# Performance work log

Measured on AMD Instinct MI355X. Metric: run time of the kernel, lower is better.

The kernel has to match this reference:

```python
import jax, jax.numpy as jnp
import numpy as np

N, E, B = 50000, 640000, 4
H, L = 128, 4
NODE_IN, EDGE_IN, COND_IN, NODE_OUT = 12, 4, 10, 3


def _mlp(x, w1, b1, w2, b2):
    # Linear -> ReLU -> Linear
    return jnp.maximum(x @ w1 + b1, 0.0) @ w2 + b2


def setup_inputs() -> dict:
    key = jax.random.key(0)
    keys = iter(jax.random.split(key, 64))

    def p(*shape):
        fan_in = shape[-2] if len(shape) >= 2 else shape[-1]
        return (jax.random.normal(next(keys), shape, jnp.float32) / np.sqrt(fan_in)).astype(jnp.float32)

    inp = {
        "x": jax.random.normal(next(keys), (N, NODE_IN), jnp.float32),
        "edge_index": jax.random.randint(next(keys), (2, E), 0, N),
        "edge_attr": jax.random.normal(next(keys), (E, EDGE_IN), jnp.float32),
        "conditions": jax.random.normal(next(keys), (B, COND_IN), jnp.float32),
        "batch": jnp.sort(jax.random.randint(next(keys), (N,), 0, B)),
        # encoders
        "enc_node_w1": p(NODE_IN, H), "enc_node_b1": jnp.zeros((H,), jnp.float32),
        "enc_node_w2": p(H, H), "enc_node_b2": jnp.zeros((H,), jnp.float32),
        "enc_edge_w1": p(EDGE_IN, H), "enc_edge_b1": jnp.zeros((H,), jnp.float32),
        "enc_edge_w2": p(H, H), "enc_edge_b2": jnp.zeros((H,), jnp.float32),
        "enc_cond_w1": p(COND_IN, H), "enc_cond_b1": jnp.zeros((H,), jnp.float32),
        "enc_cond_w2": p(H, H), "enc_cond_b2": jnp.zeros((H,), jnp.float32),
        # shared MultiheadAttention: with a single key, softmax weight == 1 per head,
        # so output = out_proj(v_proj(kv)); q/k projections cancel exactly (and have
        # identically zero gradient), so only v/out projections are materialized.
        "attn_wv": p(H, H), "attn_bv": jnp.zeros((H,), jnp.float32),
        "attn_wo": p(H, H), "attn_bo": jnp.zeros((H,), jnp.float32),
        # processor layers (stacked over L)
        "pe_w1": p(L, 4 * H, H), "pe_b1": jnp.zeros((L, H), jnp.float32),
        "pe_w2": p(L, H, H), "pe_b2": jnp.zeros((L, H), jnp.float32),
        "pn_w1": p(L, 3 * H, H), "pn_b1": jnp.zeros((L, H), jnp.float32),
        "pn_w2": p(L, H, H), "pn_b2": jnp.zeros((L, H), jnp.float32),
        # decoder
        "dec_w1": p(H, H), "dec_b1": jnp.zeros((H,), jnp.float32),
        "dec_w2": p(H, NODE_OUT), "dec_b2": jnp.zeros((NODE_OUT,), jnp.float32),
    }
    return inp


def reference(x, edge_index, edge_attr, conditions, batch,
              enc_node_w1, enc_node_b1, enc_node_w2, enc_node_b2,
              enc_edge_w1, enc_edge_b1, enc_edge_w2, enc_edge_b2,
              enc_cond_w1, enc_cond_b1, enc_cond_w2, enc_cond_b2,
              attn_wv, attn_bv, attn_wo, attn_bo,
              pe_w1, pe_b1, pe_w2, pe_b2,
              pn_w1, pn_b1, pn_w2, pn_b2,
              dec_w1, dec_b1, dec_w2, dec_b2):
    n = x.shape[0]
    h = _mlp(x, enc_node_w1, enc_node_b1, enc_node_w2, enc_node_b2)           # [N,H]
    e = _mlp(edge_attr, enc_edge_w1, enc_edge_b1, enc_edge_w2, enc_edge_b2)   # [E,H]
    u = _mlp(conditions, enc_cond_w1, enc_cond_b1, enc_cond_w2, enc_cond_b2)  # [B,H]

    row, col = edge_index[0], edge_index[1]
    u_nodes = u[batch]                                                        # [N,H]
    # single-key cross-attention -> softmax over 1 key == 1 -> out_proj(v_proj(u))
    x_cond = (u_nodes @ attn_wv + attn_bv) @ attn_wo + attn_bo               # [N,H], same every layer
    u_edges = u_nodes[row]                                                    # u[batch[row]]

    for l in range(pe_w1.shape[0]):
        # edge update: cat([src, dest, edge_attr, u[batch_e]]) -> MLP
        e = _mlp(jnp.concatenate([h[row], h[col], e, u_edges], axis=1),
                 pe_w1[l], pe_b1[l], pe_w2[l], pe_b2[l])
        # scatter-add aggregation (index_add on row)
        agg = jax.ops.segment_sum(e, row, num_segments=n)                     # [N,H]
        # node update with residual
        h = h + _mlp(jnp.concatenate([h, agg, x_cond], axis=1),
                     pn_w1[l], pn_b1[l], pn_w2[l], pn_b2[l])

    return _mlp(h, dec_w1, dec_b1, dec_w2, dec_b2)                            # [N,node_out]
```

## Files before the change

### kernel.cpp

```cpp
#include <hip/hip_runtime.h>
#include <cstddef>

#define NN 50000
#define NNP 50048
#define NE 640000
#define NB 4
#define H  128
#define NL 4
#define TE 64

typedef unsigned int u32;
typedef unsigned short u16;
typedef __attribute__((ext_vector_type(8))) short bf16x8;
typedef __attribute__((ext_vector_type(4))) float f32x4;

__device__ __forceinline__ float bf2f(u16 s) {
    union { u32 u; float f; } v; v.u = ((u32)s) << 16; return v.f;
}
__device__ __forceinline__ u16 f2bf(float f) {
    union { float f; u32 u; } v; v.f = f;
    u32 u = v.u;
    u += 0x7FFF + ((u >> 16) & 1);
    return (u16)(u >> 16);
}
__device__ __forceinline__ void unpack8(uint4 raw, float* d) {
    d[0] = bf2f(raw.x & 0xFFFF); d[1] = bf2f(raw.x >> 16);
    d[2] = bf2f(raw.y & 0xFFFF); d[3] = bf2f(raw.y >> 16);
    d[4] = bf2f(raw.z & 0xFFFF); d[5] = bf2f(raw.z >> 16);
    d[6] = bf2f(raw.w & 0xFFFF); d[7] = bf2f(raw.w >> 16);
}
__device__ __forceinline__ uint4 pack8(const float* s) {
    uint4 pk;
    pk.x = (u32)f2bf(s[0]) | ((u32)f2bf(s[1]) << 16);
    pk.y = (u32)f2bf(s[2]) | ((u32)f2bf(s[3]) << 16);
    pk.z = (u32)f2bf(s[4]) | ((u32)f2bf(s[5]) << 16);
    pk.w = (u32)f2bf(s[6]) | ((u32)f2bf(s[7]) << 16);
    return pk;
}
__device__ __forceinline__ bf16x8 ld_f32_bf8(const float* __restrict__ p) {
    const float4 a = *(const float4*)p;
    const float4 b = *(const float4*)(p + 4);
    bf16x8 r;
    r[0] = (short)f2bf(a.x); r[1] = (short)f2bf(a.y);
    r[2] = (short)f2bf(a.z); r[3] = (short)f2bf(a.w);
    r[4] = (short)f2bf(b.x); r[5] = (short)f2bf(b.y);
    r[6] = (short)f2bf(b.z); r[7] = (short)f2bf(b.w);
    return r;
}

__global__ __launch_bounds__(256) void k_zero(float* __restrict__ p, int n4) {
    const int i = blockIdx.x * 256 + threadIdx.x;
    if (i < n4) ((float4*)p)[i] = make_float4(0.f, 0.f, 0.f, 0.f);
}

__global__ __launch_bounds__(256) void k_hist(const int* __restrict__ rowi,
                                              u32* __restrict__ cnt) {
    const int i = blockIdx.x * 256 + threadIdx.x;
    if (i < NE) atomicAdd(&cnt[rowi[i]], 1u);
}

__global__ __launch_bounds__(1024) void k_scan(u32* __restrict__ cnt) {
    __shared__ u32 part[1024];
    const int t = threadIdx.x;
    const int CHUNK = (NN + 1023) / 1024;
    const int lo = t * CHUNK;
    const int hi = (lo + CHUNK < NN) ? lo + CHUNK : NN;
    u32 s = 0;
    for (int i = lo; i < hi; ++i) s += cnt[i];
    part[t] = s;
    __syncthreads();
    for (int ofs = 1; ofs < 1024; ofs <<= 1) {
        const u32 v = (t >= ofs) ? part[t - ofs] : 0u;
        __syncthreads();
        part[t] += v;
        __syncthreads();
    }
    u32 run = (t == 0) ? 0u : part[t - 1];
    for (int i = lo; i < hi; ++i) { const u32 c = cnt[i]; cnt[i] = run; run += c; }
}

__global__ __launch_bounds__(256) void k_scatter(const int* __restrict__ rowi,
                                                 const int* __restrict__ coli,
                                                 u32* __restrict__ off,
                                                 int* __restrict__ permS,
                                                 int* __restrict__ rowS,
                                                 int* __restrict__ colS) {
    const int i = blockIdx.x * 256 + threadIdx.x;
    if (i < NE) {
        const int r = rowi[i];
        const u32 p = atomicAdd(&off[r], 1u);
        permS[p] = i; rowS[p] = r; colS[p] = coli[i];
    }
}

__global__ __launch_bounds__(256) void k_prep(
    const float* __restrict__ pe_w1, const float* __restrict__ pe_w2,
    const float* __restrict__ pn_w1, const float* __restrict__ pn_w2,
    const float* __restrict__ ew2,   const float* __restrict__ nw2,
    const float* __restrict__ dw1,
    u16* __restrict__ W1t, u16* __restrict__ W2t,
    u16* __restrict__ WaT, u16* __restrict__ WbT,
    u16* __restrict__ Wn1aT, u16* __restrict__ Wn1bT, u16* __restrict__ Wn2T,
    u16* __restrict__ W2et, u16* __restrict__ W2nt, u16* __restrict__ W1dt) {
    const int li = blockIdx.x;
    const float* src; u16* dst;
    switch (blockIdx.y) {
        case 0: src = pe_w1 + ((size_t)li * 512 + 256) * H; dst = W1t  + (size_t)li * H * H; break;
        case 1: src = pe_w2 + (size_t)li * H * H;           dst = W2t  + (size_t)li * H * H; break;
        case 2: src = pe_w1 + (size_t)li * 512 * H;         dst = WaT  + (size_t)li * H * H; break;
        case 3: src = pe_w1 + ((size_t)li * 512 + 128) * H; dst = WbT  + (size_t)li * H * H; break;
        case 4: src = pn_w1 + (size_t)li * 384 * H;         dst = Wn1aT + (size_t)li * H * H; break;
        case 5: src = pn_w1 + ((size_t)li * 384 + 128) * H; dst = Wn1bT + (size_t)li * H * H; break;
        case 6: src = pn_w2 + (size_t)li * H * H;           dst = Wn2T + (size_t)li * H * H; break;
        default:
            if (li == 0)      { src = ew2; dst = W2et; }
            else if (li == 1) { src = nw2; dst = W2nt; }
            else if (li == 2) { src = dw1; dst = W1dt; }
            else return;
            break;
    }
    for (int idx = threadIdx.x; idx < H * H; idx += 256) {
        const int n = idx >> 7, k = idx & 127;
        dst[idx] = f2bf(src[(size_t)k * H + n]);
    }
}

__global__ __launch_bounds__(128) void k_small(
    const float* __restrict__ cond,
    const float* __restrict__ ecw1, const float* __restrict__ ecb1,
    const float* __restrict__ ecw2, const float* __restrict__ ecb2,
    const float* __restrict__ wv, const float* __restrict__ bv,
    const float* __restrict__ wo, const float* __restrict__ bo,
    const float* __restrict__ pe_w1, const float* __restrict__ pe_b1,
    const float* __restrict__ pn_w1, const float* __restrict__ pn_b1,
    float* __restrict__ cbat, float* __restrict__ nbat) {
    __shared__ float tmp[NB][H];
    __shared__ float uL[NB][H];
    __shared__ float xcL[NB][H];
    const int t = threadIdx.x;
    for (int b = 0; b < NB; ++b) {
        float a = ecb1[t];
        for (int k = 0; k < 10; ++k) a = fmaf(cond[b * 10 + k], ecw1[k * H + t], a);
        tmp[b][t] = fmaxf(a, 0.f);
    }
    __syncthreads();
    for (int b = 0; b < NB; ++b) {
        float a = ecb2[t];
        for (int k = 0; k < H; ++k) a = fmaf(tmp[b][k], ecw2[k * H + t], a);
        uL[b][t] = a;
    }
    __syncthreads();
    for (int b = 0; b < NB; ++b) {
        float a = bv[t];
        for (int k = 0; k < H; ++k) a = fmaf(uL[b][k], wv[k * H + t], a);
        tmp[b][t] = a;
    }
    __syncthreads();
    for (int b = 0; b < NB; ++b) {
        float a = bo[t];
        for (int k = 0; k < H; ++k) a = fmaf(tmp[b][k], wo[k * H + t], a);
        xcL[b][t] = a;
    }
    __syncthreads();
    for (int l = 0; l < NL; ++l) {
        const float* w1u = pe_w1 + ((size_t)l * 512 + 384) * H;
        for (int b = 0; b < NB; ++b) {
            float a = pe_b1[l * H + t];
            for (int k = 0; k < H; ++k) a = fmaf(uL[b][k], w1u[k * H + t], a);
            cbat[(l * NB + b) * H + t] = a;
        }
        const float* w1x = pn_w1 + ((size_t)l * 384 + 256) * H;
        for (int b = 0; b < NB; ++b) {
            float a = pn_b1[l * H + t];
            for (int k = 0; k < H; ++k) a = fmaf(xcL[b][k], w1x[k * H + t], a);
            nbat[(l * NB + b) * H + t] = a;
        }
    }
}

__global__ __launch_bounds__(256) void k_enc_e_mfma(
    const float* __restrict__ ea,
    const int* __restrict__ permS,
    const float* __restrict__ w1, const float* __restrict__ b1,
    const u16* __restrict__ W2et, const float* __restrict__ b2,
    u16* __restrict__ e) {
    __shared__ float SI[TE][H + 4];
    const int t = threadIdx.x;
    const long long e0 = (long long)blockIdx.x * TE;
    const int w = t >> 6, l = t & 63;
    const int m16 = l & 15, g = l >> 4;
    const int row = w * 16 + m16;

    const int src = permS[e0 + row];
    const float4 av = *(const float4*)&ea[(size_t)src * 4];

    bf16x8 afrag[4];
#pragma unroll
    for (int ks = 0; ks < 4; ++ks) {
        const int c0 = ks * 32 + g * 8;
        float hv[8];
        {
            const float4 ba = *(const float4*)&b1[c0];
            const float4 bb = *(const float4*)&b1[c0 + 4];
            hv[0] = ba.x; hv[1] = ba.y; hv[2] = ba.z; hv[3] = ba.w;
            hv[4] = bb.x; hv[5] = bb.y; hv[6] = bb.z; hv[7] = bb.w;
        }
#pragma unroll
        for (int k = 0; k < 4; ++k) {
            const float s = (k == 0) ? av.x : (k == 1) ? av.y : (k == 2) ? av.z : av.w;
            const float4 wa = *(const float4*)&w1[k * H + c0];
            const float4 wb = *(const float4*)&w1[k * H + c0 + 4];
            hv[0] = fmaf(s, wa.x, hv[0]); hv[1] = fmaf(s, wa.y, hv[1]);
            hv[2] = fmaf(s, wa.z, hv[2]); hv[3] = fmaf(s, wa.w, hv[3]);
            hv[4] = fmaf(s, wb.x, hv[4]); hv[5] = fmaf(s, wb.y, hv[5]);
            hv[6] = fmaf(s, wb.z, hv[6]); hv[7] = fmaf(s, wb.w, hv[7]);
        }
#pragma unroll
        for (int j = 0; j < 8; ++j) afrag[ks][j] = (short)f2bf(fmaxf(hv[j], 0.f));
    }

    f32x4 acc[8];
#pragma unroll
    for (int nt = 0; nt < 8; ++nt) {
        const float bb = b2[nt * 16 + m16];
        acc[nt][0] = bb; acc[nt][1] = bb; acc[nt][2] = bb; acc[nt][3] = bb;
    }
#pragma unroll
    for (int ks = 0; ks < 4; ++ks) {
#pragma unroll
        for (int nt = 0; nt < 8; ++nt) {
            const bf16x8 bfr =
                *(const bf16x8*)&W2et[(size_t)(nt * 16 + m16) * H + ks * 32 + g * 8];
            acc[nt] = __builtin_amdgcn_mfma_f32_16x16x32_bf16(afrag[ks], bfr, acc[nt], 0, 0, 0);
        }
    }

#pragma unroll
    for (int nt = 0; nt < 8; ++nt)
#pragma unroll
        for (int j = 0; j < 4; ++j)
            SI[w * 16 + g * 4 + j][nt * 16 + m16] = acc[nt][j];
    __syncthreads();
    for (int u = t; u < TE * 16; u += 256) {
        const int j = u >> 4, c8 = (u & 15) * 8;
        *(uint4*)&e[(size_t)(e0 + j) * H + c8] = pack8(&SI[j][c8]);
    }
}

__global__ __launch_bounds__(256) void k_enc_n_mfma(
    const float* __restrict__ x,
    const float* __restrict__ w1, const float* __restrict__ b1,
    const u16* __restrict__ W2nt, const float* __restrict__ b2,
    float* __restrict__ h) {
    __shared__ float SI[TE][H + 4];
    const int t = threadIdx.x;
    const long long n0 = (long long)blockIdx.x * TE;
    const int w = t >> 6, l = t & 63;
    const int m16 = l & 15, g = l >> 4;
    const int row = w * 16 + m16;
    const long long nr = (n0 + row < NN) ? (n0 + row) : (NN - 1);

    float av[12];
    {
        const float4 a0 = *(const float4*)&x[nr * 12];
        const float4 a1 = *(const float4*)&x[nr * 12 + 4];
        const float4 a2 = *(const float4*)&x[nr * 12 + 8];
        av[0] = a0.x; av[1] = a0.y; av[2] = a0.z; av[3] = a0.w;
        av[4] = a1.x; av[5] = a1.y; av[6] = a1.z; av[7] = a1.w;
        av[8] = a2.x; av[9] = a2.y; av[10] = a2.z; av[11] = a2.w;
    }

    bf16x8 afrag[4];
#pragma unroll
    for (int ks = 0; ks < 4; ++ks) {
        const int c0 = ks * 32 + g * 8;
        float hv[8];
        {
            const float4 ba = *(const float4*)&b1[c0];
            const float4 bb = *(const float4*)&b1[c0 + 4];
            hv[0] = ba.x; hv[1] = ba.y; hv[2] = ba.z; hv[3] = ba.w;
            hv[4] = bb.x; hv[5] = bb.y; hv[6] = bb.z; hv[7] = bb.w;
        }
#pragma unroll
        for (int k = 0; k < 12; ++k) {
            const float s = av[k];
            const float4 wa = *(const float4*)&w1[k * H + c0];
            const float4 wb = *(const float4*)&w1[k * H + c0 + 4];
            hv[0] = fmaf(s, wa.x, hv[0]); hv[1] = fmaf(s, wa.y, hv[1]);
            hv[2] = fmaf(s, wa.z, hv[2]); hv[3] = fmaf(s, wa.w, hv[3]);
            hv[4] = fmaf(s, wb.x, hv[4]); hv[5] = fmaf(s, wb.y, hv[5]);
            hv[6] = fmaf(s, wb.z, hv[6]); hv[7] = fmaf(s, wb.w, hv[7]);
        }
#pragma unroll
        for (int j = 0; j < 8; ++j) afrag[ks][j] = (short)f2bf(fmaxf(hv[j], 0.f));
    }

    f32x4 acc[8];
#pragma unroll
    for (int nt = 0; nt < 8; ++nt) {
        const float bb = b2[nt * 16 + m16];
        acc[nt][0] = bb; acc[nt][1] = bb; acc[nt][2] = bb; acc[nt][3] = bb;
    }
#pragma unroll
    for (int ks = 0; ks < 4; ++ks) {
#pragma unroll
        for (int nt = 0; nt < 8; ++nt) {
            const bf16x8 bfr =
                *(const bf16x8*)&W2nt[(size_t)(nt * 16 + m16) * H + ks * 32 + g * 8];
            acc[nt] = __builtin_amdgcn_mfma_f32_16x16x32_bf16(afrag[ks], bfr, acc[nt], 0, 0, 0);
        }
    }

#pragma unroll
    for (int nt = 0; nt < 8; ++nt)
#pragma unroll
        for (int j = 0; j < 4; ++j)
            SI[w * 16 + g * 4 + j][nt * 16 + m16] = acc[nt][j];
    __syncthreads();
    for (int u = t; u < TE * H / 4; u += 256) {
        const int j = u >> 5, c4 = (u & 31) * 4;
        *(float4*)&h[(size_t)(n0 + j) * H + c4] = *(const float4*)&SI[j][c4];
    }
}

__global__ __launch_bounds__(256) void k_gemm_dual_mfma(
    const float* __restrict__ h,
    const u16* __restrict__ WaT, const u16* __restrict__ WbT,
    u16* __restrict__ Ca, u16* __restrict__ Cb) {
    __shared__ u16 SI[TE][H + 8];
    const int t = threadIdx.x;
    const long long n0 = (long long)blockIdx.x * TE;
    const int w = t >> 6, l = t & 63;
    const int m16 = l & 15, g = l >> 4;
    const int row = w * 16 + m16;

    bf16x8 afrag[4];
    {
        const float* hp = h + (size_t)(n0 + row) * H + g * 8;
#pragma unroll
        for (int ks = 0; ks < 4; ++ks) afrag[ks] = ld_f32_bf8(hp + ks * 32);
    }

    f32x4 accA[8], accB[8];
#pragma unroll
    for (int nt = 0; nt < 8; ++nt) {
        accA[nt][0] = 0.f; accA[nt][1] = 0.f; accA[nt][2] = 0.f; accA[nt][3] = 0.f;
        accB[nt][0] = 0.f; accB[nt][1] = 0.f; accB[nt][2] = 0.f; accB[nt][3] = 0.f;
    }
#pragma unroll
    for (int ks = 0; ks < 4; ++ks) {
#pragma unroll
        for (int nt = 0; nt < 8; ++nt) {
            const size_t off = (size_t)(nt * 16 + m16) * H + ks * 32 + g * 8;
            const bf16x8 ba = *(const bf16x8*)&WaT[off];
            const bf16x8 bb = *(const bf16x8*)&WbT[off];
            accA[nt] = __builtin_amdgcn_mfma_f32_16x16x32_bf16(afrag[ks], ba, accA[nt], 0, 0, 0);
            accB[nt] = __builtin_amdgcn_mfma_f32_16x16x32_bf16(afrag[ks], bb, accB[nt], 0, 0, 0);
        }
    }

#pragma unroll
    for (int s = 0; s < 2; ++s) {
        __syncthreads();
#pragma unroll
        for (int nt = 0; nt < 8; ++nt)
#pragma unroll
            for (int j = 0; j < 4; ++j)
                SI[w * 16 + g * 4 + j][nt * 16 + m16] =
                    f2bf(s ? accB[nt][j] : accA[nt][j]);
        __syncthreads();
        u16* C = s ? Cb : Ca;
        for (int u = t; u < TE * 16; u += 256) {
            const int j = u >> 4, c8 = (u & 15) * 8;
            *(uint4*)&C[(size_t)(n0 + j) * H + c8] = *(const uint4*)&SI[j][c8];
        }
    }
}

template <bool WRITE_E>
__global__ __launch_bounds__(256) void k_edge_mfma(
    const u16* __restrict__ hA, const u16* __restrict__ hB,
    const float* __restrict__ cbatl,
    const u16* __restrict__ W1t, const u16* __restrict__ W2t,
    const float* __restrict__ b2,
    const int* __restrict__ rowS, const int* __restrict__ colS,
    const int* __restrict__ batch,
    u16* __restrict__ e, float* __restrict__ agg) {
    __shared__ u16 SI[TE][H + 8];
    __shared__ int rL[TE], cL[TE], bL[TE];
    const int t = threadIdx.x;
    const long long e0 = (long long)blockIdx.x * TE;
    const int w = t >> 6, l = t & 63;
    const int m16 = l & 15, g = l >> 4;

    bf16x8 afrag[4];
    {
        const u16* ep = e + (size_t)(e0 + w * 16 + m16) * H + g * 8;
#pragma unroll
        for (int ks = 0; ks < 4; ++ks) afrag[ks] = *(const bf16x8*)(ep + ks * 32);
    }

    if (t < TE) {
        const int r = rowS[e0 + t];
        rL[t] = r; cL[t] = colS[e0 + t]; bL[t] = batch[r];
    }
    __syncthreads();

    for (int u = t; u < TE * 16; u += 256) {
        const int j = u >> 4, c8 = (u & 15) * 8;
        float va[8], vb[8], sm[8];
        unpack8(*(const uint4*)&hA[(size_t)rL[j] * H + c8], va);
        unpack8(*(const uint4*)&hB[(size_t)cL[j] * H + c8], vb);
        const float* cb = &cbatl[bL[j] * H + c8];
#pragma unroll
        for (int q = 0; q < 8; ++q) sm[q] = va[q] + vb[q] + cb[q];
        *(uint4*)&SI[j][c8] = pack8(sm);
    }
    __syncthreads();

    f32x4 acc[8];
#pragma unroll
    for (int nt = 0; nt < 8; ++nt) {
#pragma unroll
        for (int j = 0; j < 4; ++j)
            acc[nt][j] = bf2f(SI[w * 16 + g * 4 + j][nt * 16 + m16]);
#pragma unroll
        for (int ks = 0; ks < 4; ++ks) {
            const bf16x8 bfr =
                *(const bf16x8*)&W1t[(size_t)(nt * 16 + m16) * H + ks * 32 + g * 8];
            acc[nt] = __builtin_amdgcn_mfma_f32_16x16x32_bf16(afrag[ks], bfr, acc[nt], 0, 0, 0);
        }
    }
    __syncthreads();

#pragma unroll
    for (int nt = 0; nt < 8; ++nt)
#pragma unroll
        for (int j = 0; j < 4; ++j)
            SI[w * 16 + g * 4 + j][nt * 16 + m16] = f2bf(fmaxf(acc[nt][j], 0.f));
    __syncthreads();

    f32x4 acc2[8];
#pragma unroll
    for (int nt = 0; nt < 8; ++nt) {
        const float bb = b2[nt * 16 + m16];
        acc2[nt][0] = bb; acc2[nt][1] = bb; acc2[nt][2] = bb; acc2[nt][3] = bb;
    }
#pragma unroll
    for (int ks = 0; ks < 4; ++ks) {
        const bf16x8 a2 = *(const bf16x8*)&SI[w * 16 + m16][ks * 32 + g * 8];
#pragma unroll
        for (int nt = 0; nt < 8; ++nt) {
            const bf16x8 bfr =
                *(const bf16x8*)&W2t[(size_t)(nt * 16 + m16) * H + ks * 32 + g * 8];
            acc2[nt] = __builtin_amdgcn_mfma_f32_16x16x32_bf16(a2, bfr, acc2[nt], 0, 0, 0);
        }
    }

    if (WRITE_E) {
        __syncthreads();
#pragma unroll
        for (int nt = 0; nt < 8; ++nt)
#pragma unroll
            for (int j = 0; j < 4; ++j)
                SI[w * 16 + g * 4 + j][nt * 16 + m16] = f2bf(acc2[nt][j]);
        __syncthreads();
        for (int u = t; u < TE * 16; u += 256) {
            const int j = u >> 4, c8 = (u & 15) * 8;
            *(uint4*)&e[(size_t)(e0 + j) * H + c8] = *(const uint4*)&SI[j][c8];
        }
    }

    {
        const int base = w * 16 + g * 4;
        const int r0 = rL[base], r1 = rL[base + 1], r2 = rL[base + 2], r3 = rL[base + 3];
#pragma unroll
        for (int nt = 0; nt < 8; ++nt) {
            const int c = nt * 16 + m16;
            float s = acc2[nt][0];
            int prev = r0;
            if (r1 == prev) s += acc2[nt][1];
            else { atomicAdd(&agg[(size_t)prev * H + c], s); s = acc2[nt][1]; prev = r1; }
            if (r2 == prev) s += acc2[nt][2];
            else { atomicAdd(&agg[(size_t)prev * H + c], s); s = acc2[nt][2]; prev = r2; }
            if (r3 == prev) s += acc2[nt][3];
            else { atomicAdd(&agg[(size_t)prev * H + c], s); s = acc2[nt][3]; prev = r3; }
            atomicAdd(&agg[(size_t)prev * H + c], s);
        }
    }
}

__global__ __launch_bounds__(256) void k_node_mfma(
    const u16* __restrict__ Wn1aT, const u16* __restrict__ Wn1bT,
    const u16* __restrict__ Wn2T, const float* __restrict__ bn2,
    const float* __restrict__ nbatl, const int* __restrict__ batch,
    const float* __restrict__ agg, float* __restrict__ h) {
    __shared__ float SI[TE][H + 4];
    __shared__ float NBl[NB][H];
    __shared__ int bL[TE];
    const int t = threadIdx.x;
    const long long n0 = (long long)blockIdx.x * TE;
    if (t < TE) {
        const long long n = n0 + t;
        bL[t] = batch[n < NN ? n : (NN - 1)];
    }
    for (int i = t; i < NB * H; i += 256) ((float*)NBl)[i] = nbatl[i];

    const int w = t >> 6, l = t & 63;
    const int m16 = l & 15, g = l >> 4;
    const int row = w * 16 + m16;

    bf16x8 afrag[4];
    {
        const float* hp = h + (size_t)(n0 + row) * H + g * 8;
#pragma unroll
        for (int ks = 0; ks < 4; ++ks) afrag[ks] = ld_f32_bf8(hp + ks * 32);
    }
    __syncthreads();

    f32x4 acc[8];
#pragma unroll
    for (int nt = 0; nt < 8; ++nt)
#pragma unroll
        for (int j = 0; j < 4; ++j)
            acc[nt][j] = NBl[bL[w * 16 + g * 4 + j]][nt * 16 + m16];

#pragma unroll
    for (int ks = 0; ks < 4; ++ks)
#pragma unroll
        for (int nt = 0; nt < 8; ++nt) {
            const bf16x8 bfr =
                *(const bf16x8*)&Wn1aT[(size_t)(nt * 16 + m16) * H + ks * 32 + g * 8];
            acc[nt] = __builtin_amdgcn_mfma_f32_16x16x32_bf16(afrag[ks], bfr, acc[nt], 0, 0, 0);
        }

    {
        const float* ap = agg + (size_t)(n0 + row) * H + g * 8;
#pragma unroll
        for (int ks = 0; ks < 4; ++ks) afrag[ks] = ld_f32_bf8(ap + ks * 32);
    }
#pragma unroll
    for (int ks = 0; ks < 4; ++ks)
#pragma unroll
        for (int nt = 0; nt < 8; ++nt) {
            const bf16x8 bfr =
                *(const bf16x8*)&Wn1bT[(size_t)(nt * 16 + m16) * H + ks * 32 + g * 8];
            acc[nt] = __builtin_amdgcn_mfma_f32_16x16x32_bf16(afrag[ks], bfr, acc[nt], 0, 0, 0);
        }

#pragma unroll
    for (int nt = 0; nt < 8; ++nt)
#pragma unroll
        for (int j = 0; j < 4; ++j)
            SI[w * 16 + g * 4 + j][nt * 16 + m16] = fmaxf(acc[nt][j], 0.f);
    __syncthreads();

    f32x4 acc2[8];
#pragma unroll
    for (int nt = 0; nt < 8; ++nt) {
        const float bb = bn2[nt * 16 + m16];
        acc2[nt][0] = bb; acc2[nt][1] = bb; acc2[nt][2] = bb; acc2[nt][3] = bb;
    }
#pragma unroll
    for (int ks = 0; ks < 4; ++ks) {
        bf16x8 a2;
        const float* hp = &SI[w * 16 + m16][ks * 32 + g * 8];
#pragma unroll
        for (int j = 0; j < 8; ++j) a2[j] = (short)f2bf(hp[j]);
#pragma unroll
        for (int nt = 0; nt < 8; ++nt) {
            const bf16x8 bfr =
                *(const bf16x8*)&Wn2T[(size_t)(nt * 16 + m16) * H + ks * 32 + g * 8];
            acc2[nt] = __builtin_amdgcn_mfma_f32_16x16x32_bf16(a2, bfr, acc2[nt], 0, 0, 0);
        }
    }
    __syncthreads();

#pragma unroll
    for (int nt = 0; nt < 8; ++nt)
#pragma unroll
        for (int j = 0; j < 4; ++j)
            SI[w * 16 + g * 4 + j][nt * 16 + m16] = acc2[nt][j];
    __syncthreads();

    for (int u = t; u < TE * H / 4; u += 256) {
        const int j = u >> 5, c4 = (u & 31) * 4;
        float4 hv = *(const float4*)&h[(size_t)(n0 + j) * H + c4];
        const float4 sv = *(const float4*)&SI[j][c4];
        hv.x += sv.x; hv.y += sv.y; hv.z += sv.z; hv.w += sv.w;
        *(float4*)&h[(size_t)(n0 + j) * H + c4] = hv;
    }
}

__global__ __launch_bounds__(256) void k_dec_mfma(
    const float* __restrict__ h,
    const u16* __restrict__ W1dt, const float* __restrict__ b1,
    const float* __restrict__ w2, const float* __restrict__ b2,
    float* __restrict__ out) {
    __shared__ float SI[TE][H + 4];
    const int t = threadIdx.x;
    const long long n0 = (long long)blockIdx.x * TE;
    const int w = t >> 6, l = t & 63;
    const int m16 = l & 15, g = l >> 4;
    const int row = w * 16 + m16;

    bf16x8 afrag[4];
    {
        const float* hp = h + (size_t)(n0 + row) * H + g * 8;
#pragma unroll
        for (int ks = 0; ks < 4; ++ks) afrag[ks] = ld_f32_bf8(hp + ks * 32);
    }

    f32x4 acc[8];
#pragma unroll
    for (int nt = 0; nt < 8; ++nt) {
        const float bb = b1[nt * 16 + m16];
        acc[nt][0] = bb; acc[nt][1] = bb; acc[nt][2] = bb; acc[nt][3] = bb;
    }
#pragma unroll
    for (int ks = 0; ks < 4; ++ks) {
#pragma unroll
        for (int nt = 0; nt < 8; ++nt) {
            const bf16x8 bfr =
                *(const bf16x8*)&W1dt[(size_t)(nt * 16 + m16) * H + ks * 32 + g * 8];
            acc[nt] = __builtin_amdgcn_mfma_f32_16x16x32_bf16(afrag[ks], bfr, acc[nt], 0, 0, 0);
        }
    }

#pragma unroll
    for (int nt = 0; nt < 8; ++nt)
#pragma unroll
        for (int j = 0; j < 4; ++j)
            SI[w * 16 + g * 4 + j][nt * 16 + m16] = fmaxf(acc[nt][j], 0.f);
    __syncthreads();

    if (t < TE * 3) {
        const int n = t / 3, c = t - n * 3;
        if (n0 + n < NN) {
            float v = b2[c];
            for (int k = 0; k < H; ++k) v = fmaf(SI[n][k], w2[k * 3 + c], v);
            out[(size_t)(n0 + n) * 3 + c] = v;
        }
    }
}

extern "C" void kernel_launch(void* const* d_in, const int* in_sizes, int n_in,
                              void* d_out, int out_size, void* d_ws, size_t ws_size,
                              hipStream_t stream) {
    const float* x          = (const float*)d_in[0];
    const int*   edge_index = (const int*)d_in[1];
    const float* edge_attr  = (const float*)d_in[2];
    const float* cond       = (const float*)d_in[3];
    const int*   batch      = (const int*)d_in[4];
    const float* enc_node_w1 = (const float*)d_in[5];
    const float* enc_node_b1 = (const float*)d_in[6];
    const float* enc_node_w2 = (const float*)d_in[7];
    const float* enc_node_b2 = (const float*)d_in[8];
    const float* enc_edge_w1 = (const float*)d_in[9];
    const float* enc_edge_b1 = (const float*)d_in[10];
    const float* enc_edge_w2 = (const float*)d_in[11];
    const float* enc_edge_b2 = (const float*)d_in[12];
    const float* enc_cond_w1 = (const float*)d_in[13];
    const float* enc_cond_b1 = (const float*)d_in[14];
    const float* enc_cond_w2 = (const float*)d_in[15];
    const float* enc_cond_b2 = (const float*)d_in[16];
    const float* attn_wv = (const float*)d_in[17];
    const float* attn_bv = (const float*)d_in[18];
    const float* attn_wo = (const float*)d_in[19];
    const float* attn_bo = (const float*)d_in[20];
    const float* pe_w1 = (const float*)d_in[21];
    const float* pe_b1 = (const float*)d_in[22];
    const float* pe_w2 = (const float*)d_in[23];
    const float* pe_b2 = (const float*)d_in[24];
    const float* pn_w1 = (const float*)d_in[25];
    const float* pn_b1 = (const float*)d_in[26];
    const float* pn_w2 = (const float*)d_in[27];
    const float* pn_b2 = (const float*)d_in[28];
    const float* dec_w1 = (const float*)d_in[29];
    const float* dec_b1 = (const float*)d_in[30];
    const float* dec_w2 = (const float*)d_in[31];
    const float* dec_b2 = (const float*)d_in[32];

    u16*   e    = (u16*)d_ws;
    float* h    = (float*)((char*)d_ws + (size_t)NE * H * 2);
    float* agg  = h + (size_t)NNP * H;
    u16*   hA   = (u16*)(agg + (size_t)NNP * H);
    u16*   hB   = hA + (size_t)NNP * H;
    float* cbat = (float*)(hB + (size_t)NNP * H);
    float* nbat = cbat + NL * NB * H;
    u16*   W1t   = (u16*)(nbat + NL * NB * H);
    u16*   W2t   = W1t  + (size_t)NL * H * H;
    u16*   WaT   = W2t  + (size_t)NL * H * H;
    u16*   WbT   = WaT  + (size_t)NL * H * H;
    u16*   Wn1aT = WbT  + (size_t)NL * H * H;
    u16*   Wn1bT = Wn1aT + (size_t)NL * H * H;
    u16*   Wn2T  = Wn1bT + (size_t)NL * H * H;
    u16*   W2et  = Wn2T + (size_t)NL * H * H;
    u16*   W2nt  = W2et + (size_t)H * H;
    u16*   W1dt  = W2nt + (size_t)H * H;
    u32*   cnt   = (u32*)(W1dt + (size_t)H * H);
    int*   permS = (int*)(cnt + NNP);
    int*   rowS  = permS + NE;
    int*   colS  = rowS + NE;

    const int* rowi = edge_index;
    const int* coli = edge_index + NE;
    float* out = (float*)d_out;

    k_zero<<<(NNP / 4 + 255) / 256, 256, 0, stream>>>((float*)cnt, NNP / 4);
    k_hist<<<NE / 256, 256, 0, stream>>>(rowi, cnt);
    k_scan<<<1, 1024, 0, stream>>>(cnt);
    k_scatter<<<NE / 256, 256, 0, stream>>>(rowi, coli, cnt, permS, rowS, colS);

    k_prep<<<dim3(NL, 8), 256, 0, stream>>>(pe_w1, pe_w2, pn_w1, pn_w2,
                                            enc_edge_w2, enc_node_w2, dec_w1,
                                            W1t, W2t, WaT, WbT,
                                            Wn1aT, Wn1bT, Wn2T, W2et, W2nt, W1dt);
    k_small<<<1, 128, 0, stream>>>(cond, enc_cond_w1, enc_cond_b1, enc_cond_w2, enc_cond_b2,
                                   attn_wv, attn_bv, attn_wo, attn_bo,
                                   pe_w1, pe_b1, pn_w1, pn_b1, cbat, nbat);
    k_enc_n_mfma<<<NNP / TE, 256, 0, stream>>>(
        x, enc_node_w1, enc_node_b1, W2nt, enc_node_b2, h);
    k_enc_e_mfma<<<NE / TE, 256, 0, stream>>>(
        edge_attr, permS, enc_edge_w1, enc_edge_b1, W2et, enc_edge_b2, e);

    for (int l = 0; l < NL; ++l) {
        k_zero<<<(NNP * H / 4 + 255) / 256, 256, 0, stream>>>(agg, NNP * H / 4);
        k_gemm_dual_mfma<<<NNP / TE, 256, 0, stream>>>(h, WaT + (size_t)l * H * H,
                                                       WbT + (size_t)l * H * H, hA, hB);
        if (l < NL - 1)
            k_edge_mfma<true><<<NE / TE, 256, 0, stream>>>(
                hA, hB, cbat + l * NB * H,
                W1t + (size_t)l * H * H, W2t + (size_t)l * H * H,
                pe_b2 + l * H, rowS, colS, batch, e, agg);
        else
            k_edge_mfma<false><<<NE / TE, 256, 0, stream>>>(
                hA, hB, cbat + l * NB * H,
                W1t + (size_t)l * H * H, W2t + (size_t)l * H * H,
                pe_b2 + l * H, rowS, colS, batch, e, agg);
        k_node_mfma<<<NNP / TE, 256, 0, stream>>>(
            Wn1aT + (size_t)l * H * H, Wn1bT + (size_t)l * H * H,
            Wn2T + (size_t)l * H * H, pn_b2 + l * H,
            nbat + l * NB * H, batch, agg, h);
    }
    k_dec_mfma<<<NNP / TE, 256, 0, stream>>>(h, W1dt, dec_b1, dec_w2, dec_b2, out);
}
```

Measured before the change: 2.607 ms.

## Process 128 edges per block with two MFMA row tiles per wave

The edge MLP kernel now handles 128 edges per block, with each wave owning 32 rows as two 16-row MFMA tiles. Each W1t/W2t B-fragment load then feeds two MFMAs. Because each wave only touches its own LDS rows, the barriers between the GEMM stages are dropped. Row, column and batch indices are loaded into registers with an unrolled gather for more memory-level parallelism, and the scatter-add pre-combines runs of equal row over 8 rows instead of 4 before issuing atomics. The trade-off is higher register pressure, which may lower occupancy, and half as many blocks.

```diff
diff --git a/kernel.cpp b/kernel.cpp
--- a/kernel.cpp
+++ b/kernel.cpp
@@ -8,6 +8,7 @@
 #define H  128
 #define NL 4
 #define TE 64
+#define TEE 128
 
 typedef unsigned int u32;
 typedef unsigned short u16;
@@ -386,106 +387,132 @@
     const int* __restrict__ rowS, const int* __restrict__ colS,
     const int* __restrict__ batch,
     u16* __restrict__ e, float* __restrict__ agg) {
-    __shared__ u16 SI[TE][H + 8];
-    __shared__ int rL[TE], cL[TE], bL[TE];
+    __shared__ u16 SI[TEE][H + 8];
     const int t = threadIdx.x;
-    const long long e0 = (long long)blockIdx.x * TE;
+    const long long e0 = (long long)blockIdx.x * TEE;
     const int w = t >> 6, l = t & 63;
     const int m16 = l & 15, g = l >> 4;
 
-    bf16x8 afrag[4];
+    bf16x8 af0[4], af1[4];
     {
-        const u16* ep = e + (size_t)(e0 + w * 16 + m16) * H + g * 8;
-#pragma unroll
-        for (int ks = 0; ks < 4; ++ks) afrag[ks] = *(const bf16x8*)(ep + ks * 32);
-    }
-
-    if (t < TE) {
-        const int r = rowS[e0 + t];
-        rL[t] = r; cL[t] = colS[e0 + t]; bL[t] = batch[r];
-    }
-    __syncthreads();
-
-    for (int u = t; u < TE * 16; u += 256) {
-        const int j = u >> 4, c8 = (u & 15) * 8;
-        float va[8], vb[8], sm[8];
-        unpack8(*(const uint4*)&hA[(size_t)rL[j] * H + c8], va);
-        unpack8(*(const uint4*)&hB[(size_t)cL[j] * H + c8], vb);
-        const float* cb = &cbatl[bL[j] * H + c8];
-#pragma unroll
-        for (int q = 0; q < 8; ++q) sm[q] = va[q] + vb[q] + cb[q];
-        *(uint4*)&SI[j][c8] = pack8(sm);
-    }
-    __syncthreads();
-
-    f32x4 acc[8];
+        const u16* ep0 = e + (size_t)(e0 + w * 32 + m16) * H + g * 8;
+        const u16* ep1 = ep0 + 16 * H;
+#pragma unroll
+        for (int ks = 0; ks < 4; ++ks) {
+            af0[ks] = *(const bf16x8*)(ep0 + ks * 32);
+            af1[ks] = *(const bf16x8*)(ep1 + ks * 32);
+        }
+    }
+
+    {
+        int rj[8], cj[8], bj[8];
+#pragma unroll
+        for (int it = 0; it < 8; ++it) {
+            const int j = (t + it * 256) >> 4;
+            rj[it] = rowS[e0 + j];
+            cj[it] = colS[e0 + j];
+        }
+#pragma unroll
+        for (int it = 0; it < 8; ++it) bj[it] = batch[rj[it]];
+#pragma unroll
+        for (int it = 0; it < 8; ++it) {
+            const int u = t + it * 256;
+            const int j = u >> 4, c8 = (u & 15) * 8;
+            float va[8], vb[8], sm[8];
+            unpack8(*(const uint4*)&hA[(size_t)rj[it] * H + c8], va);
+            unpack8(*(const uint4*)&hB[(size_t)cj[it] * H + c8], vb);
+            const float* cb = &cbatl[bj[it] * H + c8];
+#pragma unroll
+            for (int q = 0; q < 8; ++q) sm[q] = va[q] + vb[q] + cb[q];
+            *(uint4*)&SI[j][c8] = pack8(sm);
+        }
+    }
+    __syncthreads();
+
+    f32x4 acc0[8], acc1[8];
 #pragma unroll
     for (int nt = 0; nt < 8; ++nt) {
 #pragma unroll
-        for (int j = 0; j < 4; ++j)
-            acc[nt][j] = bf2f(SI[w * 16 + g * 4 + j][nt * 16 + m16]);
-#pragma unroll
-        for (int ks = 0; ks < 4; ++ks) {
+        for (int j = 0; j < 4; ++j) {
+            acc0[nt][j] = bf2f(SI[w * 32 + g * 4 + j][nt * 16 + m16]);
+            acc1[nt][j] = bf2f(SI[w * 32 + 16 + g * 4 + j][nt * 16 + m16]);
+        }
+    }
+#pragma unroll
+    for (int ks = 0; ks < 4; ++ks) {
+#pragma unroll
+        for (int nt = 0; nt < 8; ++nt) {
             const bf16x8 bfr =
                 *(const bf16x8*)&W1t[(size_t)(nt * 16 + m16) * H + ks * 32 + g * 8];
-            acc[nt] = __builtin_amdgcn_mfma_f32_16x16x32_bf16(afrag[ks], bfr, acc[nt], 0, 0, 0);
-        }
-    }
-    __syncthreads();
+            acc0[nt] = __builtin_amdgcn_mfma_f32_16x16x32_bf16(af0[ks], bfr, acc0[nt], 0, 0, 0);
+            acc1[nt] = __builtin_amdgcn_mfma_f32_16x16x32_bf16(af1[ks], bfr, acc1[nt], 0, 0, 0);
+        }
+    }
 
 #pragma unroll
     for (int nt = 0; nt < 8; ++nt)
 #pragma unroll
-        for (int j = 0; j < 4; ++j)
-            SI[w * 16 + g * 4 + j][nt * 16 + m16] = f2bf(fmaxf(acc[nt][j], 0.f));
-    __syncthreads();
-
-    f32x4 acc2[8];
+        for (int j = 0; j < 4; ++j) {
+            SI[w * 32 + g * 4 + j][nt * 16 + m16]      = f2bf(fmaxf(acc0[nt][j], 0.f));
+            SI[w * 32 + 16 + g * 4 + j][nt * 16 + m16] = f2bf(fmaxf(acc1[nt][j], 0.f));
+        }
+
+    f32x4 ac20[8], ac21[8];
 #pragma unroll
     for (int nt = 0; nt < 8; ++nt) {
         const float bb = b2[nt * 16 + m16];
-        acc2[nt][0] = bb; acc2[nt][1] = bb; acc2[nt][2] = bb; acc2[nt][3] = bb;
-    }
-#pragma unroll
-    for (int ks = 0; ks < 4; ++ks) {
-        const bf16x8 a2 = *(const bf16x8*)&SI[w * 16 + m16][ks * 32 + g * 8];
+        ac20[nt][0] = bb; ac20[nt][1] = bb; ac20[nt][2] = bb; ac20[nt][3] = bb;
+        ac21[nt][0] = bb; ac21[nt][1] = bb; ac21[nt][2] = bb; ac21[nt][3] = bb;
+    }
+#pragma unroll
+    for (int ks = 0; ks < 4; ++ks) {
+        const bf16x8 a20 = *(const bf16x8*)&SI[w * 32 + m16][ks * 32 + g * 8];
+        const bf16x8 a21 = *(const bf16x8*)&SI[w * 32 + 16 + m16][ks * 32 + g * 8];
 #pragma unroll
         for (int nt = 0; nt < 8; ++nt) {
             const bf16x8 bfr =
                 *(const bf16x8*)&W2t[(size_t)(nt * 16 + m16) * H + ks * 32 + g * 8];
-            acc2[nt] = __builtin_amdgcn_mfma_f32_16x16x32_bf16(a2, bfr, acc2[nt], 0, 0, 0);
+            ac20[nt] = __builtin_amdgcn_mfma_f32_16x16x32_bf16(a20, bfr, ac20[nt], 0, 0, 0);
+            ac21[nt] = __builtin_amdgcn_mfma_f32_16x16x32_bf16(a21, bfr, ac21[nt], 0, 0, 0);
+        }
+    }
+
+    {
+        int r[8];
+#pragma unroll
+        for (int j = 0; j < 4; ++j) {
+            r[j]     = rowS[e0 + w * 32 + g * 4 + j];
+            r[4 + j] = rowS[e0 + w * 32 + 16 + g * 4 + j];
+        }
+#pragma unroll
+        for (int nt = 0; nt < 8; ++nt) {
+            const int c = nt * 16 + m16;
+            float v[8];
+#pragma unroll
+            for (int j = 0; j < 4; ++j) { v[j] = ac20[nt][j]; v[4 + j] = ac21[nt][j]; }
+            float s = v[0];
+            int prev = r[0];
+#pragma unroll
+            for (int j = 1; j < 8; ++j) {
+                if (r[j] == prev) s += v[j];
+                else { atomicAdd(&agg[(size_t)prev * H + c], s); s = v[j]; prev = r[j]; }
+            }
+            atomicAdd(&agg[(size_t)prev * H + c], s);
         }
     }
 
     if (WRITE_E) {
+#pragma unroll
+        for (int nt = 0; nt < 8; ++nt)
+#pragma unroll
+            for (int j = 0; j < 4; ++j) {
+                SI[w * 32 + g * 4 + j][nt * 16 + m16]      = f2bf(ac20[nt][j]);
+                SI[w * 32 + 16 + g * 4 + j][nt * 16 + m16] = f2bf(ac21[nt][j]);
+            }
         __syncthreads();
-#pragma unroll
-        for (int nt = 0; nt < 8; ++nt)
-#pragma unroll
-            for (int j = 0; j < 4; ++j)
-                SI[w * 16 + g * 4 + j][nt * 16 + m16] = f2bf(acc2[nt][j]);
-        __syncthreads();
-        for (int u = t; u < TE * 16; u += 256) {
+        for (int u = t; u < TEE * 16; u += 256) {
             const int j = u >> 4, c8 = (u & 15) * 8;
             *(uint4*)&e[(size_t)(e0 + j) * H + c8] = *(const uint4*)&SI[j][c8];
-        }
-    }
-
-    {
-        const int base = w * 16 + g * 4;
-        const int r0 = rL[base], r1 = rL[base + 1], r2 = rL[base + 2], r3 = rL[base + 3];
-#pragma unroll
-        for (int nt = 0; nt < 8; ++nt) {
-            const int c = nt * 16 + m16;
-            float s = acc2[nt][0];
-            int prev = r0;
-            if (r1 == prev) s += acc2[nt][1];
-            else { atomicAdd(&agg[(size_t)prev * H + c], s); s = acc2[nt][1]; prev = r1; }
-            if (r2 == prev) s += acc2[nt][2];
-            else { atomicAdd(&agg[(size_t)prev * H + c], s); s = acc2[nt][2]; prev = r2; }
-            if (r3 == prev) s += acc2[nt][3];
-            else { atomicAdd(&agg[(size_t)prev * H + c], s); s = acc2[nt][3]; prev = r3; }
-            atomicAdd(&agg[(size_t)prev * H + c], s);
         }
     }
 }
@@ -729,12 +756,12 @@
         k_gemm_dual_mfma<<<NNP / TE, 256, 0, stream>>>(h, WaT + (size_t)l * H * H,
                                                        WbT + (size_t)l * H * H, hA, hB);
         if (l < NL - 1)
-            k_edge_mfma<true><<<NE / TE, 256, 0, stream>>>(
+            k_edge_mfma<true><<<NE / TEE, 256, 0, stream>>>(
                 hA, hB, cbat + l * NB * H,
                 W1t + (size_t)l * H * H, W2t + (size_t)l * H * H,
                 pe_b2 + l * H, rowS, colS, batch, e, agg);
         else
-            k_edge_mfma<false><<<NE / TE, 256, 0, stream>>>(
+            k_edge_mfma<false><<<NE / TEE, 256, 0, stream>>>(
                 hA, hB, cbat + l * NB * H,
                 W1t + (size_t)l * H * H, W2t + (size_t)l * H * H,
                 pe_b2 + l * H, rowS, colS, batch, e, agg);
```

Result: faster. 2.425 ms (-7.0%).
